# Optimization experiments

Hardware: AMD Instinct MI355X
Metric: run time of the kernel (lower is better)

Reference implementation:

```python
import jax, jax.numpy as jnp
import numpy as np

TOPK = 20

def setup_inputs() -> dict:
    key = jax.random.key(0)
    k1, k2, k3 = jax.random.split(key, 3)
    B, n, D = 4, 4096, 256
    src1 = jax.random.normal(k1, (B, n, D), dtype=jnp.float32)
    src2 = jax.random.normal(k2, (B, n, D), dtype=jnp.float32)
    memoryMartix = jax.random.normal(k3, (n, n), dtype=jnp.float32)
    return {"src1": src1, "src2": src2, "memoryMartix": memoryMartix}

def reference(src1, src2, memoryMartix):
    # softmax over dim=1 of the [n, n] memory matrix
    probs = jax.nn.softmax(memoryMartix, axis=1)            # [n, n]
    # top-k along dim=1: values and indices per row
    vtopk, ind = jax.lax.top_k(probs, TOPK)                 # [n, k], [n, k]
    # gather src2 rows per output position: [B, n, k, D]
    gathered = jnp.take(src2, ind, axis=1)
    # weighted sum over the k selected neighbors
    src = jnp.einsum('bnkd,nk->bnd', gathered, vtopk)       # [B, n, D]
    return src + src1
```

## Files before the change

kernel.cpp:

```cpp
#include <hip/hip_runtime.h>
#include <math.h>

#define TOPK  20
#define NROW  4096
#define DDIM  256
#define NB    4
#define NCHUNK 16

#define AWPB   2
#define ABLOCK (AWPB * 64)
#define BBLOCK 256

typedef float vf4 __attribute__((ext_vector_type(4)));

__device__ __forceinline__ void wave_lds_fence() {
    asm volatile("s_waitcnt lgkmcnt(0)" ::: "memory");
}

__device__ __forceinline__ bool lex_gt(float av, int ai, float bv, int bi) {
    return (av > bv) || (av == bv && ai < bi);
}

__device__ __forceinline__ void bitonic64_desc(float& v, int& i, int lane) {
#pragma unroll
    for (int k = 2; k <= 64; k <<= 1) {
#pragma unroll
        for (int j = k >> 1; j > 0; j >>= 1) {
            float pv = __shfl_xor(v, j, 64);
            int   pi = __shfl_xor(i, j, 64);
            bool takeBig = ((lane & k) == 0) == ((lane & j) == 0);
            bool pBig = lex_gt(pv, pi, v, i);
            if (takeBig == pBig) { v = pv; i = pi; }
        }
    }
}

__global__ __launch_bounds__(ABLOCK, 4) void topk_select(
    const float* __restrict__ mem,
    float* __restrict__ ws_w,
    int*   __restrict__ ws_i)
{
    __shared__ float cand_v[AWPB][64];
    __shared__ int   cand_i[AWPB][64];
    const int wave = threadIdx.x >> 6;
    const int lane = threadIdx.x & 63;
    const int n    = blockIdx.x * AWPB + wave;

    const float4* mrow = (const float4*)(mem + (size_t)n * NROW);
    float4 v4[NCHUNK];
#pragma unroll
    for (int j = 0; j < NCHUNK; ++j) v4[j] = mrow[lane + 64 * j];

    float bv = -INFINITY; int bi = 0x7fffffff;
#pragma unroll
    for (int j = 0; j < NCHUNK; ++j) {
        const int base = 4 * lane + 256 * j;
        if (v4[j].x > bv) { bv = v4[j].x; bi = base + 0; }
        if (v4[j].y > bv) { bv = v4[j].y; bi = base + 1; }
        if (v4[j].z > bv) { bv = v4[j].z; bi = base + 2; }
        if (v4[j].w > bv) { bv = v4[j].w; bi = base + 3; }
    }

    float sv = bv; int si = bi;
    bitonic64_desc(sv, si, lane);
    const float rowmax = __shfl(sv, 0, 64);
    const float tv     = __shfl(sv, 19, 64);
    const int   ti     = __shfl(si, 19, 64);

    float lsum = 0.f;
#pragma unroll
    for (int j = 0; j < NCHUNK; ++j) {
        lsum += __expf(v4[j].x - rowmax) + __expf(v4[j].y - rowmax)
              + __expf(v4[j].z - rowmax) + __expf(v4[j].w - rowmax);
    }
#pragma unroll
    for (int o = 32; o > 0; o >>= 1) lsum += __shfl_xor(lsum, o, 64);
    const float inv_denom = 1.0f / lsum;

    int cnt = 0;
#pragma unroll
    for (int j = 0; j < NCHUNK; ++j) {
        const int base = 4 * lane + 256 * j;
        cnt += (v4[j].x > tv) || (v4[j].x == tv && (base + 0) <= ti);
        cnt += (v4[j].y > tv) || (v4[j].y == tv && (base + 1) <= ti);
        cnt += (v4[j].z > tv) || (v4[j].z == tv && (base + 2) <= ti);
        cnt += (v4[j].w > tv) || (v4[j].w == tv && (base + 3) <= ti);
    }
    int incl = cnt;
#pragma unroll
    for (int o = 1; o < 64; o <<= 1) {
        int t = __shfl_up(incl, o, 64);
        if (lane >= o) incl += t;
    }
    const int total = __builtin_amdgcn_readfirstlane(__shfl(incl, 63, 64));

    float* gw = ws_w + (size_t)n * TOPK;
    int*   gi = ws_i + (size_t)n * TOPK;

    if (total <= 64) {
        int off = incl - cnt;
#pragma unroll
        for (int j = 0; j < NCHUNK; ++j) {
            const int base = 4 * lane + 256 * j;
            const float4 q = v4[j];
            if ((q.x > tv) || (q.x == tv && (base + 0) <= ti)) { cand_v[wave][off] = q.x; cand_i[wave][off] = base + 0; ++off; }
            if ((q.y > tv) || (q.y == tv && (base + 1) <= ti)) { cand_v[wave][off] = q.y; cand_i[wave][off] = base + 1; ++off; }
            if ((q.z > tv) || (q.z == tv && (base + 2) <= ti)) { cand_v[wave][off] = q.z; cand_i[wave][off] = base + 2; ++off; }
            if ((q.w > tv) || (q.w == tv && (base + 3) <= ti)) { cand_v[wave][off] = q.w; cand_i[wave][off] = base + 3; ++off; }
        }
        wave_lds_fence();
        float cv = -INFINITY; int ci = 0x7fffffff;
        if (lane < total) { cv = cand_v[wave][lane]; ci = cand_i[wave][lane]; }
        bitonic64_desc(cv, ci, lane);
        if (lane < TOPK) {
            gw[lane] = __expf(cv - rowmax) * inv_denom;
            gi[lane] = ci;
        }
    } else {
        unsigned long long dead = 0;
        float cv = bv; int ci = bi;
        for (int r = 0; r < TOPK; ++r) {
            float wv = cv; int wi = ci;
#pragma unroll
            for (int o = 32; o > 0; o >>= 1) {
                float ov = __shfl_xor(wv, o, 64);
                int   oi = __shfl_xor(wi, o, 64);
                if (lex_gt(ov, oi, wv, wi)) { wv = ov; wi = oi; }
            }
            if (lane == 0) {
                gw[r] = __expf(wv - rowmax) * inv_denom;
                gi[r] = wi;
            }
            if (ci == wi) {
                const int e = 4 * ((wi >> 8) & 15) + (wi & 3);
                dead |= (1ull << e);
                cv = -INFINITY; ci = 0x7fffffff;
#pragma unroll
                for (int j = 0; j < NCHUNK; ++j) {
                    const int base = 4 * lane + 256 * j;
                    if (!((dead >> (4 * j + 0)) & 1) && v4[j].x > cv) { cv = v4[j].x; ci = base + 0; }
                    if (!((dead >> (4 * j + 1)) & 1) && v4[j].y > cv) { cv = v4[j].y; ci = base + 1; }
                    if (!((dead >> (4 * j + 2)) & 1) && v4[j].z > cv) { cv = v4[j].z; ci = base + 2; }
                    if (!((dead >> (4 * j + 3)) & 1) && v4[j].w > cv) { cv = v4[j].w; ci = base + 3; }
                }
            }
        }
    }
}

__global__ __launch_bounds__(BBLOCK, 4) void gather_epilogue(
    const float* __restrict__ src1,
    const float* __restrict__ src2,
    const float* __restrict__ ws_w,
    const int*   __restrict__ ws_i,
    float* __restrict__ out)
{
    const int bid    = blockIdx.x;
    const int b      = (bid & 7) >> 1;
    const int ngroup = ((bid >> 3) << 1) | (bid & 1);
    const int wave   = threadIdx.x >> 6;
    const int lane   = threadIdx.x & 63;
    const int n      = ngroup * 4 + wave;

    const float* gw = ws_w + (size_t)n * TOPK;
    const int*   gi = ws_i + (size_t)n * TOPK;
    float wk[TOPK]; int ik[TOPK];
#pragma unroll
    for (int k = 0; k < TOPK; ++k) { wk[k] = gw[k]; ik[k] = gi[k]; }

    const vf4* s1  = (const vf4*)src1;
    const vf4* s2b = (const vf4*)src2 + (size_t)b * NROW * (DDIM / 4);
    vf4*       o4  = (vf4*)out;

    const size_t rowbase = ((size_t)b * NROW + n) * (DDIM / 4) + lane;
    vf4 acc = __builtin_nontemporal_load(s1 + rowbase);
#pragma unroll
    for (int k = 0; k < TOPK; ++k) {
        const vf4 g = s2b[(size_t)ik[k] * (DDIM / 4) + lane];
        acc += wk[k] * g;
    }
    __builtin_nontemporal_store(acc, o4 + rowbase);
}

extern "C" void kernel_launch(void* const* d_in, const int* in_sizes, int n_in,
                              void* d_out, int out_size, void* d_ws, size_t ws_size,
                              hipStream_t stream) {
    const float* src1 = (const float*)d_in[0];
    const float* src2 = (const float*)d_in[1];
    const float* mem  = (const float*)d_in[2];
    float* out = (float*)d_out;

    float* ws_w = (float*)d_ws;
    int*   ws_i = (int*)d_ws + (size_t)NROW * TOPK;

    topk_select<<<NROW / AWPB, ABLOCK, 0, stream>>>(mem, ws_w, ws_i);
    gather_epilogue<<<NROW, BBLOCK, 0, stream>>>(src1, src2, ws_w, ws_i, out);
}
```

Baseline: 152.1 us.

## Fuse top-k selection and gather epilogue into one kernel via LDS

Merges the two kernels into one. Each wave computes the softmax top-k for one row and writes the weights and indices to shared memory. After a block barrier, each wave handles one batch and runs the weighted gather for all four rows of the block. This removes a kernel launch and the workspace round trip through global memory. In exchange, the gather phase cannot begin until all four waves finish selection, and each block has to carry both phases' register pressure.

```diff
diff --git a/kernel.cpp b/kernel.cpp
--- a/kernel.cpp
+++ b/kernel.cpp
@@ -7,9 +7,8 @@
 #define NB    4
 #define NCHUNK 16
 
-#define AWPB   2
-#define ABLOCK (AWPB * 64)
-#define BBLOCK 256
+#define FWPB   4
+#define FBLOCK (FWPB * 64)
 
 typedef float vf4 __attribute__((ext_vector_type(4)));
 
@@ -35,151 +34,142 @@
     }
 }
 
-__global__ __launch_bounds__(ABLOCK, 4) void topk_select(
+__global__ __launch_bounds__(FBLOCK, 4) void fused_topk_gather(
+    const float* __restrict__ src1,
+    const float* __restrict__ src2,
     const float* __restrict__ mem,
-    float* __restrict__ ws_w,
-    int*   __restrict__ ws_i)
+    float* __restrict__ out)
 {
-    __shared__ float cand_v[AWPB][64];
-    __shared__ int   cand_i[AWPB][64];
+    __shared__ float cand_v[FWPB][64];
+    __shared__ int   cand_i[FWPB][64];
+    __shared__ float sw[FWPB][TOPK];
+    __shared__ int   si_[FWPB][TOPK];
+
     const int wave = threadIdx.x >> 6;
     const int lane = threadIdx.x & 63;
-    const int n    = blockIdx.x * AWPB + wave;
+    const int n    = blockIdx.x * FWPB + wave;
 
-    const float4* mrow = (const float4*)(mem + (size_t)n * NROW);
-    float4 v4[NCHUNK];
+    {
+        const float4* mrow = (const float4*)(mem + (size_t)n * NROW);
+        float4 v4[NCHUNK];
 #pragma unroll
-    for (int j = 0; j < NCHUNK; ++j) v4[j] = mrow[lane + 64 * j];
+        for (int j = 0; j < NCHUNK; ++j) v4[j] = mrow[lane + 64 * j];
 
-    float bv = -INFINITY; int bi = 0x7fffffff;
-#pragma unroll
-    for (int j = 0; j < NCHUNK; ++j) {
-        const int base = 4 * lane + 256 * j;
-        if (v4[j].x > bv) { bv = v4[j].x; bi = base + 0; }
-        if (v4[j].y > bv) { bv = v4[j].y; bi = base + 1; }
-        if (v4[j].z > bv) { bv = v4[j].z; bi = base + 2; }
-        if (v4[j].w > bv) { bv = v4[j].w; bi = base + 3; }
-    }
-
-    float sv = bv; int si = bi;
-    bitonic64_desc(sv, si, lane);
-    const float rowmax = __shfl(sv, 0, 64);
-    const float tv     = __shfl(sv, 19, 64);
-    const int   ti     = __shfl(si, 19, 64);
-
-    float lsum = 0.f;
-#pragma unroll
-    for (int j = 0; j < NCHUNK; ++j) {
-        lsum += __expf(v4[j].x - rowmax) + __expf(v4[j].y - rowmax)
-              + __expf(v4[j].z - rowmax) + __expf(v4[j].w - rowmax);
-    }
-#pragma unroll
-    for (int o = 32; o > 0; o >>= 1) lsum += __shfl_xor(lsum, o, 64);
-    const float inv_denom = 1.0f / lsum;
-
-    int cnt = 0;
-#pragma unroll
-    for (int j = 0; j < NCHUNK; ++j) {
-        const int base = 4 * lane + 256 * j;
-        cnt += (v4[j].x > tv) || (v4[j].x == tv && (base + 0) <= ti);
-        cnt += (v4[j].y > tv) || (v4[j].y == tv && (base + 1) <= ti);
-        cnt += (v4[j].z > tv) || (v4[j].z == tv && (base + 2) <= ti);
-        cnt += (v4[j].w > tv) || (v4[j].w == tv && (base + 3) <= ti);
-    }
-    int incl = cnt;
-#pragma unroll
-    for (int o = 1; o < 64; o <<= 1) {
-        int t = __shfl_up(incl, o, 64);
-        if (lane >= o) incl += t;
-    }
-    const int total = __builtin_amdgcn_readfirstlane(__shfl(incl, 63, 64));
-
-    float* gw = ws_w + (size_t)n * TOPK;
-    int*   gi = ws_i + (size_t)n * TOPK;
-
-    if (total <= 64) {
-        int off = incl - cnt;
+        float bv = -INFINITY; int bi = 0x7fffffff;
 #pragma unroll
         for (int j = 0; j < NCHUNK; ++j) {
             const int base = 4 * lane + 256 * j;
-            const float4 q = v4[j];
-            if ((q.x > tv) || (q.x == tv && (base + 0) <= ti)) { cand_v[wave][off] = q.x; cand_i[wave][off] = base + 0; ++off; }
-            if ((q.y > tv) || (q.y == tv && (base + 1) <= ti)) { cand_v[wave][off] = q.y; cand_i[wave][off] = base + 1; ++off; }
-            if ((q.z > tv) || (q.z == tv && (base + 2) <= ti)) { cand_v[wave][off] = q.z; cand_i[wave][off] = base + 2; ++off; }
-            if ((q.w > tv) || (q.w == tv && (base + 3) <= ti)) { cand_v[wave][off] = q.w; cand_i[wave][off] = base + 3; ++off; }
+            if (v4[j].x > bv) { bv = v4[j].x; bi = base + 0; }
+            if (v4[j].y > bv) { bv = v4[j].y; bi = base + 1; }
+            if (v4[j].z > bv) { bv = v4[j].z; bi = base + 2; }
+            if (v4[j].w > bv) { bv = v4[j].w; bi = base + 3; }
         }
-        wave_lds_fence();
-        float cv = -INFINITY; int ci = 0x7fffffff;
-        if (lane < total) { cv = cand_v[wave][lane]; ci = cand_i[wave][lane]; }
-        bitonic64_desc(cv, ci, lane);
-        if (lane < TOPK) {
-            gw[lane] = __expf(cv - rowmax) * inv_denom;
-            gi[lane] = ci;
+
+        float sv = bv; int si = bi;
+        bitonic64_desc(sv, si, lane);
+        const float rowmax = __shfl(sv, 0, 64);
+        const float tv     = __shfl(sv, 19, 64);
+        const int   ti     = __shfl(si, 19, 64);
+
+        float lsum = 0.f;
+#pragma unroll
+        for (int j = 0; j < NCHUNK; ++j) {
+            lsum += __expf(v4[j].x - rowmax) + __expf(v4[j].y - rowmax)
+                  + __expf(v4[j].z - rowmax) + __expf(v4[j].w - rowmax);
         }
-    } else {
-        unsigned long long dead = 0;
-        float cv = bv; int ci = bi;
-        for (int r = 0; r < TOPK; ++r) {
-            float wv = cv; int wi = ci;
 #pragma unroll
-            for (int o = 32; o > 0; o >>= 1) {
-                float ov = __shfl_xor(wv, o, 64);
-                int   oi = __shfl_xor(wi, o, 64);
-                if (lex_gt(ov, oi, wv, wi)) { wv = ov; wi = oi; }
+        for (int o = 32; o > 0; o >>= 1) lsum += __shfl_xor(lsum, o, 64);
+        const float inv_denom = 1.0f / lsum;
+
+        int cnt = 0;
+#pragma unroll
+        for (int j = 0; j < NCHUNK; ++j) {
+            const int base = 4 * lane + 256 * j;
+            cnt += (v4[j].x > tv) || (v4[j].x == tv && (base + 0) <= ti);
+            cnt += (v4[j].y > tv) || (v4[j].y == tv && (base + 1) <= ti);
+            cnt += (v4[j].z > tv) || (v4[j].z == tv && (base + 2) <= ti);
+            cnt += (v4[j].w > tv) || (v4[j].w == tv && (base + 3) <= ti);
+        }
+        int incl = cnt;
+#pragma unroll
+        for (int o = 1; o < 64; o <<= 1) {
+            int t = __shfl_up(incl, o, 64);
+            if (lane >= o) incl += t;
+        }
+        const int total = __builtin_amdgcn_readfirstlane(__shfl(incl, 63, 64));
+
+        if (total <= 64) {
+            int off = incl - cnt;
+#pragma unroll
+            for (int j = 0; j < NCHUNK; ++j) {
+                const int base = 4 * lane + 256 * j;
+                const float4 q = v4[j];
+                if ((q.x > tv) || (q.x == tv && (base + 0) <= ti)) { cand_v[wave][off] = q.x; cand_i[wave][off] = base + 0; ++off; }
+                if ((q.y > tv) || (q.y == tv && (base + 1) <= ti)) { cand_v[wave][off] = q.y; cand_i[wave][off] = base + 1; ++off; }
+                if ((q.z > tv) || (q.z == tv && (base + 2) <= ti)) { cand_v[wave][off] = q.z; cand_i[wave][off] = base + 2; ++off; }
+                if ((q.w > tv) || (q.w == tv && (base + 3) <= ti)) { cand_v[wave][off] = q.w; cand_i[wave][off] = base + 3; ++off; }
             }
-            if (lane == 0) {
-                gw[r] = __expf(wv - rowmax) * inv_denom;
-                gi[r] = wi;
+            wave_lds_fence();
+            float cv = -INFINITY; int ci = 0x7fffffff;
+            if (lane < total) { cv = cand_v[wave][lane]; ci = cand_i[wave][lane]; }
+            bitonic64_desc(cv, ci, lane);
+            if (lane < TOPK) {
+                sw[wave][lane]  = __expf(cv - rowmax) * inv_denom;
+                si_[wave][lane] = ci;
             }
-            if (ci == wi) {
-                const int e = 4 * ((wi >> 8) & 15) + (wi & 3);
-                dead |= (1ull << e);
-                cv = -INFINITY; ci = 0x7fffffff;
+        } else {
+            unsigned long long dead = 0;
+            float cv = bv; int ci = bi;
+            for (int r = 0; r < TOPK; ++r) {
+                float wv = cv; int wi = ci;
 #pragma unroll
-                for (int j = 0; j < NCHUNK; ++j) {
-                    const int base = 4 * lane + 256 * j;
-                    if (!((dead >> (4 * j + 0)) & 1) && v4[j].x > cv) { cv = v4[j].x; ci = base + 0; }
-                    if (!((dead >> (4 * j + 1)) & 1) && v4[j].y > cv) { cv = v4[j].y; ci = base + 1; }
-                    if (!((dead >> (4 * j + 2)) & 1) && v4[j].z > cv) { cv = v4[j].z; ci = base + 2; }
-                    if (!((dead >> (4 * j + 3)) & 1) && v4[j].w > cv) { cv = v4[j].w; ci = base + 3; }
+                for (int o = 32; o > 0; o >>= 1) {
+                    float ov = __shfl_xor(wv, o, 64);
+                    int   oi = __shfl_xor(wi, o, 64);
+                    if (lex_gt(ov, oi, wv, wi)) { wv = ov; wi = oi; }
+                }
+                if (lane == 0) {
+                    sw[wave][r]  = __expf(wv - rowmax) * inv_denom;
+                    si_[wave][r] = wi;
+                }
+                if (ci == wi) {
+                    const int e = 4 * ((wi >> 8) & 15) + (wi & 3);
+                    dead |= (1ull << e);
+                    cv = -INFINITY; ci = 0x7fffffff;
+#pragma unroll
+                    for (int j = 0; j < NCHUNK; ++j) {
+                        const int base = 4 * lane + 256 * j;
+                        if (!((dead >> (4 * j + 0)) & 1) && v4[j].x > cv) { cv = v4[j].x; ci = base + 0; }
+                        if (!((dead >> (4 * j + 1)) & 1) && v4[j].y > cv) { cv = v4[j].y; ci = base + 1; }
+                        if (!((dead >> (4 * j + 2)) & 1) && v4[j].z > cv) { cv = v4[j].z; ci = base + 2; }
+                        if (!((dead >> (4 * j + 3)) & 1) && v4[j].w > cv) { cv = v4[j].w; ci = base + 3; }
+                    }
                 }
             }
         }
     }
-}
 
-__global__ __launch_bounds__(BBLOCK, 4) void gather_epilogue(
-    const float* __restrict__ src1,
-    const float* __restrict__ src2,
-    const float* __restrict__ ws_w,
-    const int*   __restrict__ ws_i,
-    float* __restrict__ out)
-{
-    const int bid    = blockIdx.x;
-    const int b      = (bid & 7) >> 1;
-    const int ngroup = ((bid >> 3) << 1) | (bid & 1);
-    const int wave   = threadIdx.x >> 6;
-    const int lane   = threadIdx.x & 63;
-    const int n      = ngroup * 4 + wave;
+    __syncthreads();
 
-    const float* gw = ws_w + (size_t)n * TOPK;
-    const int*   gi = ws_i + (size_t)n * TOPK;
-    float wk[TOPK]; int ik[TOPK];
+    const int b = wave;
+    const vf4* s2b = (const vf4*)src2 + (size_t)b * NROW * (DDIM / 4);
+
 #pragma unroll
-    for (int k = 0; k < TOPK; ++k) { wk[k] = gw[k]; ik[k] = gi[k]; }
+    for (int r = 0; r < FWPB; ++r) {
+        const int nr = blockIdx.x * FWPB + r;
+        float wk[TOPK]; int ik[TOPK];
+#pragma unroll
+        for (int k = 0; k < TOPK; ++k) { wk[k] = sw[r][k]; ik[k] = si_[r][k]; }
 
-    const vf4* s1  = (const vf4*)src1;
-    const vf4* s2b = (const vf4*)src2 + (size_t)b * NROW * (DDIM / 4);
-    vf4*       o4  = (vf4*)out;
-
-    const size_t rowbase = ((size_t)b * NROW + n) * (DDIM / 4) + lane;
-    vf4 acc = __builtin_nontemporal_load(s1 + rowbase);
+        const size_t rowbase = ((size_t)b * NROW + nr) * (DDIM / 4) + lane;
+        vf4 acc = __builtin_nontemporal_load((const vf4*)src1 + rowbase);
 #pragma unroll
-    for (int k = 0; k < TOPK; ++k) {
-        const vf4 g = s2b[(size_t)ik[k] * (DDIM / 4) + lane];
-        acc += wk[k] * g;
+        for (int k = 0; k < TOPK; ++k) {
+            const vf4 g = s2b[(size_t)ik[k] * (DDIM / 4) + lane];
+            acc += wk[k] * g;
+        }
+        __builtin_nontemporal_store(acc, (vf4*)out + rowbase);
     }
-    __builtin_nontemporal_store(acc, o4 + rowbase);
 }
 
 extern "C" void kernel_launch(void* const* d_in, const int* in_sizes, int n_in,
@@ -189,10 +179,7 @@
     const float* src2 = (const float*)d_in[1];
     const float* mem  = (const float*)d_in[2];
     float* out = (float*)d_out;
+    (void)d_ws; (void)ws_size;
 
-    float* ws_w = (float*)d_ws;
-    int*   ws_i = (int*)d_ws + (size_t)NROW * TOPK;
-
-    topk_select<<<NROW / AWPB, ABLOCK, 0, stream>>>(mem, ws_w, ws_i);
-    gather_epilogue<<<NROW, BBLOCK, 0, stream>>>(src1, src2, ws_w, ws_i, out);
+    fused_topk_gather<<<NROW / FWPB, FBLOCK, 0, stream>>>(src1, src2, mem, out);
 }
```

Result: slower. 161.8 us (+6.3%).
